# Optimization experiments

Measured on AMD Instinct MI355X. Metric: run time of the kernel, lower is better.

## Reference

```python
import jax, jax.numpy as jnp
import numpy as np

IN_FEATURES = 1024
OUT_FEATURES = 256
BATCH = 131072
EPS = 1e-4


def setup_inputs() -> dict:
    key = jax.random.key(0)
    kx, kw, kb = jax.random.split(key, 3)
    x = jax.random.normal(kx, (BATCH, IN_FEATURES), dtype=jnp.float32)
    # nn.Linear default init: U(-1/sqrt(in), 1/sqrt(in)) for both W and b
    bound = 1.0 / np.sqrt(IN_FEATURES)
    W = jax.random.uniform(kw, (OUT_FEATURES, IN_FEATURES), dtype=jnp.float32, minval=-bound, maxval=bound)
    b = jax.random.uniform(kb, (OUT_FEATURES,), dtype=jnp.float32, minval=-bound, maxval=bound)
    return {"x": x, "W": W, "b": b}


def reference(x, W, b):
    # L2-normalize each row (dim=1), matching x / (||x||_2 + 1e-4)
    norm = jnp.sqrt(jnp.sum(x * x, axis=1, keepdims=True))
    x_dir = x / (norm + EPS)
    # Linear: x_dir @ W^T + b, then ReLU
    h = jnp.einsum('bi,oi->bo', x_dir, W) + b
    return jax.nn.relu(h)
```

## Files before the change

kernel.cpp:

```cpp
#include <hip/hip_runtime.h>


#define IN_F   1024
#define OUT_F  256
#define BATCH  131072
#define BM     128
#define NKT    32
#define EPSV   1e-4f

typedef __attribute__((ext_vector_type(8))) __bf16 bf16x8;
typedef __attribute__((ext_vector_type(4))) __bf16 bf16x4;
typedef __attribute__((ext_vector_type(4))) float  f32x4;

__device__ __forceinline__ void gload_lds16(const void* g, void* lds) {
  __builtin_amdgcn_global_load_lds(
      (const __attribute__((address_space(1))) void*)g,
      (__attribute__((address_space(3))) void*)lds, 16, 0, 0);
}

#define VM_WAIT(N) do { asm volatile("s_waitcnt vmcnt(" #N ")" ::: "memory"); \
                        __builtin_amdgcn_sched_barrier(0); } while (0)

__global__ void wconv_kernel(const float* __restrict__ W, __bf16* __restrict__ Wb) {
  const int t = blockIdx.x * blockDim.x + threadIdx.x;
  const float4 v = reinterpret_cast<const float4*>(W)[t];
  bf16x4 h;
  h[0] = (__bf16)v.x; h[1] = (__bf16)v.y; h[2] = (__bf16)v.z; h[3] = (__bf16)v.w;
  reinterpret_cast<bf16x4*>(Wb)[t] = h;
}

__global__ __launch_bounds__(1024, 4)
void ffl_kernel(const float* __restrict__ x, const __bf16* __restrict__ Wb,
                const float* __restrict__ bias, float* __restrict__ out) {
  __shared__ __align__(16) char smem[163840];
  char* const Ab[3] = {smem, smem + 32768, smem + 65536};
  char* const Bb[4] = {smem + 98304, smem + 114688, smem + 131072, smem + 147456};

  const int tid  = threadIdx.x;
  const int lane = tid & 63;
  const int wave = tid >> 6;
  const int wr   = wave >> 2;
  const int wc   = wave & 3;
  const int rm   = lane & 15;
  const int q    = lane >> 4;
  const size_t block_row = (size_t)blockIdx.x * BM;
  const int phg = blockIdx.x & 15;

  const float* aSrc[2]; int aDst[2];
  #pragma unroll
  for (int i = 0; i < 2; ++i) {
    const int c   = 2 * wave + i;
    const int row = 4 * c + (lane >> 4);
    const int s   = (lane & 15) ^ (row & 7);
    aSrc[i] = x + (block_row + row) * IN_F + s * 4;
    aDst[i] = c * 1024;
  }
  const int brow = 16 * wave + (lane >> 2);
  const int bs   = (lane & 3) ^ ((brow >> 1) & 3);
  const __bf16* bSrc = Wb + (size_t)brow * IN_F + bs * 8;
  const int bDst = wave * 1024;

  f32x4 acc[2][4];
  #pragma unroll
  for (int m = 0; m < 2; ++m)
    #pragma unroll
    for (int n = 0; n < 4; ++n)
      acc[m][n] = (f32x4){0.f, 0.f, 0.f, 0.f};

  float ssq0 = 0.f, ssq1 = 0.f;

  auto stageA = [&](int g) {
    const int pg = (g + phg) & 15;
    gload_lds16(aSrc[0] + pg * 64, Ab[g % 3] + aDst[0]);
    gload_lds16(aSrc[1] + pg * 64, Ab[g % 3] + aDst[1]);
  };
  auto stageB = [&](int kt) {
    const int pk = (kt + 2 * phg) & 31;
    gload_lds16(bSrc + pk * 32, Bb[kt & 3] + bDst);
  };

  stageA(0);
  stageA(1);
  stageB(0);
  stageB(1);
  stageB(2);
  VM_WAIT(2);
  __builtin_amdgcn_s_barrier();

  #pragma unroll
  for (int kt = 0; kt < NKT; ++kt) {
    if (kt + 3 < NKT) stageB(kt + 3);
    if ((kt & 1) == 0 && (kt / 2 + 2) < 16) stageA(kt / 2 + 2);

    const char* abuf = Ab[(kt >> 1) % 3];
    const char* bbuf = Bb[kt & 3];
    const int   gb   = (kt & 1) * 8 + 2 * q;

    bf16x8 aF[2];
    #pragma unroll
    for (int m = 0; m < 2; ++m) {
      const int ra = wr * 32 + m * 16 + rm;
      const char* ab = abuf + ra * 256;
      const int sw = ra & 7;
      const f32x4 lo = *reinterpret_cast<const f32x4*>(ab + ((gb)     ^ sw) * 16);
      const f32x4 hi = *reinterpret_cast<const f32x4*>(ab + ((gb + 1) ^ sw) * 16);
      float& ssq = m ? ssq1 : ssq0;
      ssq += lo[0]*lo[0] + lo[1]*lo[1] + lo[2]*lo[2] + lo[3]*lo[3]
           + hi[0]*hi[0] + hi[1]*hi[1] + hi[2]*hi[2] + hi[3]*hi[3];
      bf16x8 a;
      a[0]=(__bf16)lo[0]; a[1]=(__bf16)lo[1]; a[2]=(__bf16)lo[2]; a[3]=(__bf16)lo[3];
      a[4]=(__bf16)hi[0]; a[5]=(__bf16)hi[1]; a[6]=(__bf16)hi[2]; a[7]=(__bf16)hi[3];
      aF[m] = a;
    }

    #pragma unroll
    for (int n = 0; n < 4; ++n) {
      const int rb = wc * 64 + n * 16 + rm;
      const bf16x8 bF = *reinterpret_cast<const bf16x8*>(
          bbuf + rb * 64 + (q ^ ((rb >> 1) & 3)) * 16);
      acc[0][n] = __builtin_amdgcn_mfma_f32_16x16x32_bf16(aF[0], bF, acc[0][n], 0, 0, 0);
      acc[1][n] = __builtin_amdgcn_mfma_f32_16x16x32_bf16(aF[1], bF, acc[1][n], 0, 0, 0);
    }

    if (kt == 29)                              { VM_WAIT(1); }
    else if (kt >= 30)                         { VM_WAIT(0); }
    else if (kt == 0 || kt == 28 || (kt & 1))  { VM_WAIT(4); }
    else                                       { VM_WAIT(6); }
    __builtin_amdgcn_s_barrier();
  }

  ssq0 += __shfl_xor(ssq0, 16); ssq0 += __shfl_xor(ssq0, 32);
  ssq1 += __shfl_xor(ssq1, 16); ssq1 += __shfl_xor(ssq1, 32);
  float* norms = reinterpret_cast<float*>(smem + 163328);
  if (wc == 0 && q == 0) {
    norms[wr * 32 + rm]      = 1.0f / (sqrtf(ssq0) + EPSV);
    norms[wr * 32 + 16 + rm] = 1.0f / (sqrtf(ssq1) + EPSV);
  }
  __syncthreads();

  float* stg = reinterpret_cast<float*>(smem);
  const int col0 = wc * 64 + rm;
  #pragma unroll
  for (int n = 0; n < 4; ++n) {
    const float bn = bias[col0 + n * 16];
    #pragma unroll
    for (int m = 0; m < 2; ++m) {
      #pragma unroll
      for (int j = 0; j < 4; ++j) {
        const int lr = wr * 32 + m * 16 + q * 4 + j;
        stg[lr * 260 + col0 + n * 16] = fmaxf(acc[m][n][j] * norms[lr] + bn, 0.f);
      }
    }
  }
  __syncthreads();

  const int r = tid >> 3, p = tid & 7;
  const float* srow = stg + r * 260;
  float* orow = out + (block_row + r) * OUT_F;
  #pragma unroll
  for (int i = 0; i < 8; ++i) {
    const int f = i * 8 + p;
    const f32x4 v = *reinterpret_cast<const f32x4*>(srow + f * 4);
    *reinterpret_cast<f32x4*>(orow + f * 4) = v;
  }
}

extern "C" void kernel_launch(void* const* d_in, const int* in_sizes, int n_in,
                              void* d_out, int out_size, void* d_ws, size_t ws_size,
                              hipStream_t stream) {
  const float* x = (const float*)d_in[0];
  const float* W = (const float*)d_in[1];
  const float* b = (const float*)d_in[2];
  float* out = (float*)d_out;
  __bf16* Wb = (__bf16*)d_ws;

  wconv_kernel<<<(OUT_F * IN_F / 4) / 256, 256, 0, stream>>>(W, Wb);
  ffl_kernel<<<BATCH / BM, 1024, 0, stream>>>(x, Wb, b, out);
}
```

Baseline: 170.6 us.

## Halve block to 512 threads with 64x64 per-wave tiles

Cuts the workgroup from 16 to 8 waves. Each wave now covers 64 rows by 64 columns, holding 4x4 accumulators, and issues twice as many async global-to-LDS loads per stage. The wait counts are retuned to match. The goal is fewer LDS B-fragment reads per MFMA and less barrier overhead per block, at the cost of more registers per thread, which may limit occupancy. LDS use is unchanged at 160KB, so still one block per CU.

```diff
diff --git a/kernel.cpp b/kernel.cpp
--- a/kernel.cpp
+++ b/kernel.cpp
@@ -29,7 +29,7 @@
   reinterpret_cast<bf16x4*>(Wb)[t] = h;
 }
 
-__global__ __launch_bounds__(1024, 4)
+__global__ __launch_bounds__(512, 2)
 void ffl_kernel(const float* __restrict__ x, const __bf16* __restrict__ Wb,
                 const float* __restrict__ bias, float* __restrict__ out) {
   __shared__ __align__(16) char smem[163840];
@@ -46,45 +46,53 @@
   const size_t block_row = (size_t)blockIdx.x * BM;
   const int phg = blockIdx.x & 15;
 
-  const float* aSrc[2]; int aDst[2];
+  const float* aSrc[4]; int aDst[4];
   #pragma unroll
-  for (int i = 0; i < 2; ++i) {
-    const int c   = 2 * wave + i;
+  for (int i = 0; i < 4; ++i) {
+    const int c   = 4 * wave + i;
     const int row = 4 * c + (lane >> 4);
     const int s   = (lane & 15) ^ (row & 7);
     aSrc[i] = x + (block_row + row) * IN_F + s * 4;
     aDst[i] = c * 1024;
   }
-  const int brow = 16 * wave + (lane >> 2);
-  const int bs   = (lane & 3) ^ ((brow >> 1) & 3);
-  const __bf16* bSrc = Wb + (size_t)brow * IN_F + bs * 8;
-  const int bDst = wave * 1024;
+  const __bf16* bSrc[2]; int bDst[2];
+  #pragma unroll
+  for (int i = 0; i < 2; ++i) {
+    const int c    = 2 * wave + i;
+    const int brow = 16 * c + (lane >> 2);
+    const int bs   = (lane & 3) ^ ((brow >> 1) & 3);
+    bSrc[i] = Wb + (size_t)brow * IN_F + bs * 8;
+    bDst[i] = c * 1024;
+  }
 
-  f32x4 acc[2][4];
+  f32x4 acc[4][4];
   #pragma unroll
-  for (int m = 0; m < 2; ++m)
+  for (int m = 0; m < 4; ++m)
     #pragma unroll
     for (int n = 0; n < 4; ++n)
       acc[m][n] = (f32x4){0.f, 0.f, 0.f, 0.f};
 
-  float ssq0 = 0.f, ssq1 = 0.f;
+  float ssq[4] = {0.f, 0.f, 0.f, 0.f};
 
   auto stageA = [&](int g) {
     const int pg = (g + phg) & 15;
-    gload_lds16(aSrc[0] + pg * 64, Ab[g % 3] + aDst[0]);
-    gload_lds16(aSrc[1] + pg * 64, Ab[g % 3] + aDst[1]);
+    #pragma unroll
+    for (int i = 0; i < 4; ++i)
+      gload_lds16(aSrc[i] + pg * 64, Ab[g % 3] + aDst[i]);
   };
   auto stageB = [&](int kt) {
     const int pk = (kt + 2 * phg) & 31;
-    gload_lds16(bSrc + pk * 32, Bb[kt & 3] + bDst);
+    #pragma unroll
+    for (int i = 0; i < 2; ++i)
+      gload_lds16(bSrc[i] + pk * 32, Bb[kt & 3] + bDst[i]);
   };
 
   stageA(0);
+  stageB(0);
   stageA(1);
-  stageB(0);
   stageB(1);
   stageB(2);
-  VM_WAIT(2);
+  VM_WAIT(8);
   __builtin_amdgcn_s_barrier();
 
   #pragma unroll
@@ -96,17 +104,16 @@
     const char* bbuf = Bb[kt & 3];
     const int   gb   = (kt & 1) * 8 + 2 * q;
 
-    bf16x8 aF[2];
+    bf16x8 aF[4];
     #pragma unroll
-    for (int m = 0; m < 2; ++m) {
-      const int ra = wr * 32 + m * 16 + rm;
+    for (int m = 0; m < 4; ++m) {
+      const int ra = wr * 64 + m * 16 + rm;
       const char* ab = abuf + ra * 256;
       const int sw = ra & 7;
       const f32x4 lo = *reinterpret_cast<const f32x4*>(ab + ((gb)     ^ sw) * 16);
       const f32x4 hi = *reinterpret_cast<const f32x4*>(ab + ((gb + 1) ^ sw) * 16);
-      float& ssq = m ? ssq1 : ssq0;
-      ssq += lo[0]*lo[0] + lo[1]*lo[1] + lo[2]*lo[2] + lo[3]*lo[3]
-           + hi[0]*hi[0] + hi[1]*hi[1] + hi[2]*hi[2] + hi[3]*hi[3];
+      ssq[m] += lo[0]*lo[0] + lo[1]*lo[1] + lo[2]*lo[2] + lo[3]*lo[3]
+              + hi[0]*hi[0] + hi[1]*hi[1] + hi[2]*hi[2] + hi[3]*hi[3];
       bf16x8 a;
       a[0]=(__bf16)lo[0]; a[1]=(__bf16)lo[1]; a[2]=(__bf16)lo[2]; a[3]=(__bf16)lo[3];
       a[4]=(__bf16)hi[0]; a[5]=(__bf16)hi[1]; a[6]=(__bf16)hi[2]; a[7]=(__bf16)hi[3];
@@ -118,23 +125,28 @@
       const int rb = wc * 64 + n * 16 + rm;
       const bf16x8 bF = *reinterpret_cast<const bf16x8*>(
           bbuf + rb * 64 + (q ^ ((rb >> 1) & 3)) * 16);
-      acc[0][n] = __builtin_amdgcn_mfma_f32_16x16x32_bf16(aF[0], bF, acc[0][n], 0, 0, 0);
-      acc[1][n] = __builtin_amdgcn_mfma_f32_16x16x32_bf16(aF[1], bF, acc[1][n], 0, 0, 0);
+      #pragma unroll
+      for (int m = 0; m < 4; ++m)
+        acc[m][n] = __builtin_amdgcn_mfma_f32_16x16x32_bf16(aF[m], bF, acc[m][n], 0, 0, 0);
     }
 
-    if (kt == 29)                              { VM_WAIT(1); }
-    else if (kt >= 30)                         { VM_WAIT(0); }
-    else if (kt == 0 || kt == 28 || (kt & 1))  { VM_WAIT(4); }
-    else                                       { VM_WAIT(6); }
+    if (kt >= 30)                        { VM_WAIT(0); }
+    else if (kt == 29)                   { VM_WAIT(2); }
+    else if ((kt & 1) == 0 && kt >= 2 && kt <= 26) { VM_WAIT(12); }
+    else                                 { VM_WAIT(8); }
     __builtin_amdgcn_s_barrier();
   }
 
-  ssq0 += __shfl_xor(ssq0, 16); ssq0 += __shfl_xor(ssq0, 32);
-  ssq1 += __shfl_xor(ssq1, 16); ssq1 += __shfl_xor(ssq1, 32);
+  #pragma unroll
+  for (int m = 0; m < 4; ++m) {
+    ssq[m] += __shfl_xor(ssq[m], 16);
+    ssq[m] += __shfl_xor(ssq[m], 32);
+  }
   float* norms = reinterpret_cast<float*>(smem + 163328);
   if (wc == 0 && q == 0) {
-    norms[wr * 32 + rm]      = 1.0f / (sqrtf(ssq0) + EPSV);
-    norms[wr * 32 + 16 + rm] = 1.0f / (sqrtf(ssq1) + EPSV);
+    #pragma unroll
+    for (int m = 0; m < 4; ++m)
+      norms[wr * 64 + m * 16 + rm] = 1.0f / (sqrtf(ssq[m]) + EPSV);
   }
   __syncthreads();
 
@@ -144,10 +156,10 @@
   for (int n = 0; n < 4; ++n) {
     const float bn = bias[col0 + n * 16];
     #pragma unroll
-    for (int m = 0; m < 2; ++m) {
+    for (int m = 0; m < 4; ++m) {
       #pragma unroll
       for (int j = 0; j < 4; ++j) {
-        const int lr = wr * 32 + m * 16 + q * 4 + j;
+        const int lr = wr * 64 + m * 16 + q * 4 + j;
         stg[lr * 260 + col0 + n * 16] = fmaxf(acc[m][n][j] * norms[lr] + bn, 0.f);
       }
     }
@@ -155,13 +167,17 @@
   __syncthreads();
 
   const int r = tid >> 3, p = tid & 7;
-  const float* srow = stg + r * 260;
-  float* orow = out + (block_row + r) * OUT_F;
   #pragma unroll
-  for (int i = 0; i < 8; ++i) {
-    const int f = i * 8 + p;
-    const f32x4 v = *reinterpret_cast<const f32x4*>(srow + f * 4);
-    *reinterpret_cast<f32x4*>(orow + f * 4) = v;
+  for (int half = 0; half < 2; ++half) {
+    const int row = half * 64 + r;
+    const float* srow = stg + row * 260;
+    float* orow = out + (block_row + row) * OUT_F;
+    #pragma unroll
+    for (int i = 0; i < 8; ++i) {
+      const int f = i * 8 + p;
+      const f32x4 v = *reinterpret_cast<const f32x4*>(srow + f * 4);
+      *reinterpret_cast<f32x4*>(orow + f * 4) = v;
+    }
   }
 }
 
@@ -175,5 +191,5 @@
   __bf16* Wb = (__bf16*)d_ws;
 
   wconv_kernel<<<(OUT_F * IN_F / 4) / 256, 256, 0, stream>>>(W, Wb);
-  ffl_kernel<<<BATCH / BM, 1024, 0, stream>>>(x, Wb, b, out);
+  ffl_kernel<<<BATCH / BM, 512, 0, stream>>>(x, Wb, b, out);
 }
```

Result: slower. 177.6 us (+4.1%).

## Double the K-step per pipeline iteration and rebalance the LDS staging buffers

Applied to the files above, without the earlier changes.

Each main-loop iteration now covers 64 K-elements, as two MFMA sub-steps, instead of 32. That halves the number of iterations and of block-wide barriers and waitcnt points. The B operand moves from four 16 KB buffers to two 32 KB double buffers, with both halves loaded per stage, and the A and B stages now advance in lockstep. The aim is to cut synchronisation overhead in the 1024-thread block, at the cost of a shorter prefetch distance for B (one stage instead of three), which may expose more global-load latency.

```diff
diff --git a/kernel.cpp b/kernel.cpp
--- a/kernel.cpp
+++ b/kernel.cpp
@@ -5,7 +5,7 @@
 #define OUT_F  256
 #define BATCH  131072
 #define BM     128
-#define NKT    32
+#define NKT    16
 #define EPSV   1e-4f
 
 typedef __attribute__((ext_vector_type(8))) __bf16 bf16x8;
@@ -34,7 +34,7 @@
                 const float* __restrict__ bias, float* __restrict__ out) {
   __shared__ __align__(16) char smem[163840];
   char* const Ab[3] = {smem, smem + 32768, smem + 65536};
-  char* const Bb[4] = {smem + 98304, smem + 114688, smem + 131072, smem + 147456};
+  char* const Bb[2] = {smem + 98304, smem + 131072};
 
   const int tid  = threadIdx.x;
   const int lane = tid & 63;
@@ -69,63 +69,63 @@
 
   float ssq0 = 0.f, ssq1 = 0.f;
 
-  auto stageA = [&](int g) {
-    const int pg = (g + phg) & 15;
-    gload_lds16(aSrc[0] + pg * 64, Ab[g % 3] + aDst[0]);
-    gload_lds16(aSrc[1] + pg * 64, Ab[g % 3] + aDst[1]);
+  auto stageA = [&](int s) {
+    const int pg = (s + phg) & 15;
+    gload_lds16(aSrc[0] + pg * 64, Ab[s % 3] + aDst[0]);
+    gload_lds16(aSrc[1] + pg * 64, Ab[s % 3] + aDst[1]);
   };
-  auto stageB = [&](int kt) {
-    const int pk = (kt + 2 * phg) & 31;
-    gload_lds16(bSrc + pk * 32, Bb[kt & 3] + bDst);
+  auto stageB = [&](int s) {
+    const int pg = (s + phg) & 15;
+    gload_lds16(bSrc + pg * 64,      Bb[s & 1] + bDst);
+    gload_lds16(bSrc + pg * 64 + 32, Bb[s & 1] + 16384 + bDst);
   };
 
   stageA(0);
+  stageB(0);
   stageA(1);
-  stageB(0);
   stageB(1);
-  stageB(2);
-  VM_WAIT(2);
+  VM_WAIT(4);
   __builtin_amdgcn_s_barrier();
 
   #pragma unroll
   for (int kt = 0; kt < NKT; ++kt) {
-    if (kt + 3 < NKT) stageB(kt + 3);
-    if ((kt & 1) == 0 && (kt / 2 + 2) < 16) stageA(kt / 2 + 2);
+    if (kt >= 1 && kt + 1 < NKT) stageB(kt + 1);
+    if (kt + 2 < NKT) stageA(kt + 2);
 
-    const char* abuf = Ab[(kt >> 1) % 3];
-    const char* bbuf = Bb[kt & 3];
-    const int   gb   = (kt & 1) * 8 + 2 * q;
+    const char* abuf = Ab[kt % 3];
+    const char* bbuf = Bb[kt & 1];
 
-    bf16x8 aF[2];
     #pragma unroll
-    for (int m = 0; m < 2; ++m) {
-      const int ra = wr * 32 + m * 16 + rm;
-      const char* ab = abuf + ra * 256;
-      const int sw = ra & 7;
-      const f32x4 lo = *reinterpret_cast<const f32x4*>(ab + ((gb)     ^ sw) * 16);
-      const f32x4 hi = *reinterpret_cast<const f32x4*>(ab + ((gb + 1) ^ sw) * 16);
-      float& ssq = m ? ssq1 : ssq0;
-      ssq += lo[0]*lo[0] + lo[1]*lo[1] + lo[2]*lo[2] + lo[3]*lo[3]
-           + hi[0]*hi[0] + hi[1]*hi[1] + hi[2]*hi[2] + hi[3]*hi[3];
-      bf16x8 a;
-      a[0]=(__bf16)lo[0]; a[1]=(__bf16)lo[1]; a[2]=(__bf16)lo[2]; a[3]=(__bf16)lo[3];
-      a[4]=(__bf16)hi[0]; a[5]=(__bf16)hi[1]; a[6]=(__bf16)hi[2]; a[7]=(__bf16)hi[3];
-      aF[m] = a;
+    for (int kk = 0; kk < 2; ++kk) {
+      bf16x8 aF[2];
+      #pragma unroll
+      for (int m = 0; m < 2; ++m) {
+        const int ra = wr * 32 + m * 16 + rm;
+        const char* ab = abuf + ra * 256;
+        const int sw = ra & 7;
+        const int g0 = kk * 8 + 2 * q;
+        const f32x4 lo = *reinterpret_cast<const f32x4*>(ab + ((g0)     ^ sw) * 16);
+        const f32x4 hi = *reinterpret_cast<const f32x4*>(ab + ((g0 + 1) ^ sw) * 16);
+        float& ssq = m ? ssq1 : ssq0;
+        ssq += lo[0]*lo[0] + lo[1]*lo[1] + lo[2]*lo[2] + lo[3]*lo[3]
+             + hi[0]*hi[0] + hi[1]*hi[1] + hi[2]*hi[2] + hi[3]*hi[3];
+        bf16x8 a;
+        a[0]=(__bf16)lo[0]; a[1]=(__bf16)lo[1]; a[2]=(__bf16)lo[2]; a[3]=(__bf16)lo[3];
+        a[4]=(__bf16)hi[0]; a[5]=(__bf16)hi[1]; a[6]=(__bf16)hi[2]; a[7]=(__bf16)hi[3];
+        aF[m] = a;
+      }
+      const char* bhalf = bbuf + kk * 16384;
+      #pragma unroll
+      for (int n = 0; n < 4; ++n) {
+        const int rb = wc * 64 + n * 16 + rm;
+        const bf16x8 bF = *reinterpret_cast<const bf16x8*>(
+            bhalf + rb * 64 + (q ^ ((rb >> 1) & 3)) * 16);
+        acc[0][n] = __builtin_amdgcn_mfma_f32_16x16x32_bf16(aF[0], bF, acc[0][n], 0, 0, 0);
+        acc[1][n] = __builtin_amdgcn_mfma_f32_16x16x32_bf16(aF[1], bF, acc[1][n], 0, 0, 0);
+      }
     }
 
-    #pragma unroll
-    for (int n = 0; n < 4; ++n) {
-      const int rb = wc * 64 + n * 16 + rm;
-      const bf16x8 bF = *reinterpret_cast<const bf16x8*>(
-          bbuf + rb * 64 + (q ^ ((rb >> 1) & 3)) * 16);
-      acc[0][n] = __builtin_amdgcn_mfma_f32_16x16x32_bf16(aF[0], bF, acc[0][n], 0, 0, 0);
-      acc[1][n] = __builtin_amdgcn_mfma_f32_16x16x32_bf16(aF[1], bF, acc[1][n], 0, 0, 0);
-    }
-
-    if (kt == 29)                              { VM_WAIT(1); }
-    else if (kt >= 30)                         { VM_WAIT(0); }
-    else if (kt == 0 || kt == 28 || (kt & 1))  { VM_WAIT(4); }
-    else                                       { VM_WAIT(6); }
+    if (kt < 14) { VM_WAIT(2); } else { VM_WAIT(0); }
     __builtin_amdgcn_s_barrier();
   }
 
```

New measurement: 172.6 us. About the same (+1.1%).

## Convert A tile to bf16 once per k-step into shared buffer, dedupe norm work

Applied to the files above, without the earlier changes.

Before, each of the four column-waves converted the same fp32 A fragments to bf16 and accumulated squared norms, so that work was done four times over. Now every thread converts one float4 of the A tile to bf16 into a dedicated shared buffer, accumulates a per-thread partial sum of squares, and the MFMA loop reads bf16 fragments from that buffer. This needs an extra mid-iteration barrier per k-step and trims the B ring from four buffers to three, which shortens the prefetch depth. Row norms are then reduced from per-thread partials through shared memory.

```diff
diff --git a/kernel.cpp b/kernel.cpp
--- a/kernel.cpp
+++ b/kernel.cpp
@@ -20,6 +20,9 @@
 
 #define VM_WAIT(N) do { asm volatile("s_waitcnt vmcnt(" #N ")" ::: "memory"); \
                         __builtin_amdgcn_sched_barrier(0); } while (0)
+#define MIDBAR()   do { asm volatile("s_waitcnt lgkmcnt(0)" ::: "memory"); \
+                        __builtin_amdgcn_sched_barrier(0); \
+                        __builtin_amdgcn_s_barrier(); } while (0)
 
 __global__ void wconv_kernel(const float* __restrict__ W, __bf16* __restrict__ Wb) {
   const int t = blockIdx.x * blockDim.x + threadIdx.x;
@@ -32,9 +35,10 @@
 __global__ __launch_bounds__(1024, 4)
 void ffl_kernel(const float* __restrict__ x, const __bf16* __restrict__ Wb,
                 const float* __restrict__ bias, float* __restrict__ out) {
-  __shared__ __align__(16) char smem[163840];
+  __shared__ __align__(16) char smem[160256];
   char* const Ab[3] = {smem, smem + 32768, smem + 65536};
-  char* const Bb[4] = {smem + 98304, smem + 114688, smem + 131072, smem + 147456};
+  char* const Abf   = smem + 98304;
+  char* const Bb[3] = {smem + 106496, smem + 122880, smem + 139264};
 
   const int tid  = threadIdx.x;
   const int lane = tid & 63;
@@ -60,6 +64,10 @@
   const __bf16* bSrc = Wb + (size_t)brow * IN_F + bs * 8;
   const int bDst = wave * 1024;
 
+  const int prow = 8 * wave + ((tid & 63) >> 3);
+  const int pgs  = tid & 7;
+  const int p1_wr_byte = prow * 64 + (((pgs >> 1) ^ (prow & 3)) * 16) + (pgs & 1) * 8;
+
   f32x4 acc[2][4];
   #pragma unroll
   for (int m = 0; m < 2; ++m)
@@ -67,7 +75,7 @@
     for (int n = 0; n < 4; ++n)
       acc[m][n] = (f32x4){0.f, 0.f, 0.f, 0.f};
 
-  float ssq0 = 0.f, ssq1 = 0.f;
+  float pssq = 0.f;
 
   auto stageA = [&](int g) {
     const int pg = (g + phg) & 15;
@@ -76,65 +84,65 @@
   };
   auto stageB = [&](int kt) {
     const int pk = (kt + 2 * phg) & 31;
-    gload_lds16(bSrc + pk * 32, Bb[kt & 3] + bDst);
+    gload_lds16(bSrc + pk * 32, Bb[kt % 3] + bDst);
   };
 
   stageA(0);
+  stageB(0);
   stageA(1);
-  stageB(0);
   stageB(1);
-  stageB(2);
-  VM_WAIT(2);
+  VM_WAIT(3);
   __builtin_amdgcn_s_barrier();
 
   #pragma unroll
   for (int kt = 0; kt < NKT; ++kt) {
-    if (kt + 3 < NKT) stageB(kt + 3);
+    if (kt + 2 < NKT) stageB(kt + 2);
     if ((kt & 1) == 0 && (kt / 2 + 2) < 16) stageA(kt / 2 + 2);
 
-    const char* abuf = Ab[(kt >> 1) % 3];
-    const char* bbuf = Bb[kt & 3];
-    const int   gb   = (kt & 1) * 8 + 2 * q;
+    {
+      const char* abuf = Ab[(kt >> 1) % 3];
+      const int sg = (kt & 1) * 8 + pgs;
+      const f32x4 v = *reinterpret_cast<const f32x4*>(
+          abuf + prow * 256 + ((sg ^ (prow & 7)) * 16));
+      pssq += v[0]*v[0] + v[1]*v[1] + v[2]*v[2] + v[3]*v[3];
+      bf16x4 hb;
+      hb[0] = (__bf16)v[0]; hb[1] = (__bf16)v[1];
+      hb[2] = (__bf16)v[2]; hb[3] = (__bf16)v[3];
+      *reinterpret_cast<bf16x4*>(Abf + p1_wr_byte) = hb;
+    }
+    MIDBAR();
 
     bf16x8 aF[2];
     #pragma unroll
     for (int m = 0; m < 2; ++m) {
       const int ra = wr * 32 + m * 16 + rm;
-      const char* ab = abuf + ra * 256;
-      const int sw = ra & 7;
-      const f32x4 lo = *reinterpret_cast<const f32x4*>(ab + ((gb)     ^ sw) * 16);
-      const f32x4 hi = *reinterpret_cast<const f32x4*>(ab + ((gb + 1) ^ sw) * 16);
-      float& ssq = m ? ssq1 : ssq0;
-      ssq += lo[0]*lo[0] + lo[1]*lo[1] + lo[2]*lo[2] + lo[3]*lo[3]
-           + hi[0]*hi[0] + hi[1]*hi[1] + hi[2]*hi[2] + hi[3]*hi[3];
-      bf16x8 a;
-      a[0]=(__bf16)lo[0]; a[1]=(__bf16)lo[1]; a[2]=(__bf16)lo[2]; a[3]=(__bf16)lo[3];
-      a[4]=(__bf16)hi[0]; a[5]=(__bf16)hi[1]; a[6]=(__bf16)hi[2]; a[7]=(__bf16)hi[3];
-      aF[m] = a;
+      aF[m] = *reinterpret_cast<const bf16x8*>(
+          Abf + ra * 64 + ((q ^ (ra & 3)) * 16));
     }
-
     #pragma unroll
     for (int n = 0; n < 4; ++n) {
       const int rb = wc * 64 + n * 16 + rm;
       const bf16x8 bF = *reinterpret_cast<const bf16x8*>(
-          bbuf + rb * 64 + (q ^ ((rb >> 1) & 3)) * 16);
+          Bb[kt % 3] + rb * 64 + ((q ^ ((rb >> 1) & 3)) * 16));
       acc[0][n] = __builtin_amdgcn_mfma_f32_16x16x32_bf16(aF[0], bF, acc[0][n], 0, 0, 0);
       acc[1][n] = __builtin_amdgcn_mfma_f32_16x16x32_bf16(aF[1], bF, acc[1][n], 0, 0, 0);
     }
 
-    if (kt == 29)                              { VM_WAIT(1); }
-    else if (kt >= 30)                         { VM_WAIT(0); }
-    else if (kt == 0 || kt == 28 || (kt & 1))  { VM_WAIT(4); }
-    else                                       { VM_WAIT(6); }
+    if (kt <= 27)      { VM_WAIT(3); }
+    else if (kt <= 29) { VM_WAIT(1); }
+    else               { VM_WAIT(0); }
     __builtin_amdgcn_s_barrier();
   }
 
-  ssq0 += __shfl_xor(ssq0, 16); ssq0 += __shfl_xor(ssq0, 32);
-  ssq1 += __shfl_xor(ssq1, 16); ssq1 += __shfl_xor(ssq1, 32);
-  float* norms = reinterpret_cast<float*>(smem + 163328);
-  if (wc == 0 && q == 0) {
-    norms[wr * 32 + rm]      = 1.0f / (sqrtf(ssq0) + EPSV);
-    norms[wr * 32 + 16 + rm] = 1.0f / (sqrtf(ssq1) + EPSV);
+  float* partials = reinterpret_cast<float*>(smem + 155648);
+  partials[pgs * 128 + prow] = pssq;
+  __syncthreads();
+  float* norms = reinterpret_cast<float*>(smem + 159744);
+  if (tid < 128) {
+    float s = 0.f;
+    #pragma unroll
+    for (int g = 0; g < 8; ++g) s += partials[g * 128 + tid];
+    norms[tid] = 1.0f / (sqrtf(s) + EPSV);
   }
   __syncthreads();
 
```

Result: no change. 170.1 us, median of 2 (-0.3%).
